# Performance work log

Hardware: AMD Instinct MI355X
Metric: run time of the kernel (lower is better)

## Reference

```python
import jax, jax.numpy as jnp
import numpy as np
from jax import lax

NEG = -1e30  # safe -inf surrogate (avoids inf-inf NaNs under vjp)


def setup_inputs() -> dict:
    key = jax.random.key(0)
    k1, k2, k3, k4 = jax.random.split(key, 4)
    B, T, U, V = 8, 128, 64, 1024
    acts = jax.random.normal(k1, (B, T, U + 1, V), dtype=jnp.float32)
    # labels in [1, V): blank (0) never appears in target sequences
    labels = jax.random.randint(k2, (B, U), 1, V, dtype=jnp.int32)
    act_lens = jax.random.randint(k3, (B,), T // 2, T + 1, dtype=jnp.int32)
    label_lens = jax.random.randint(k4, (B,), U // 2, U + 1, dtype=jnp.int32)
    return {"acts": acts, "labels": labels, "act_lens": act_lens, "label_lens": label_lens}


def _rnnt_costs(acts, labels, act_lens, label_lens, blank=0):
    """Per-example negative log-likelihood of the RNNT alignment lattice.
    acts: (B, T, U+1, V) logits (warp_rnnt applies log_softmax internally).
    """
    B, T, U1, V = acts.shape
    U = U1 - 1
    lp = jax.nn.log_softmax(acts, axis=-1)
    lp_blank = lp[..., blank]                                        # (B, T, U+1)
    lab = jnp.broadcast_to(labels[:, None, :, None], (B, T, U, 1))
    lp_label = jnp.take_along_axis(lp[:, :, :U, :], lab, axis=3)[..., 0]  # (B, T, U)
    # mask label emissions beyond each example's label length
    umask = jnp.arange(U)[None, :] < label_lens[:, None]             # (B, U)
    lp_label = jnp.where(umask[:, None, :], lp_label, NEG)

    def compute_row(fb, lt):
        # fb: (B, U+1) alpha[t-1, u] + lp_blank[t-1, u] (the "from below" term)
        # lt: (B, U)   label log-probs at time t
        # new[u] = logaddexp(fb[u], new[u-1] + lt[u-1])  -- sequential in u
        def u_step(carry, x):
            fb_u, lt_u = x
            new = jnp.logaddexp(fb_u, carry + lt_u)
            return new, new
        _, rest = lax.scan(u_step, fb[:, 0], (fb[:, 1:].T, lt.T))    # (U, B)
        return jnp.concatenate([fb[:, 0:1], rest.T], axis=1)         # (B, U+1)

    # t = 0 row: alpha[0,0] = 0; only label transitions along u
    fb0 = jnp.concatenate([jnp.zeros((B, 1), acts.dtype), jnp.full((B, U), NEG, acts.dtype)], axis=1)
    row0 = compute_row(fb0, lp_label[:, 0, :])

    def t_step(prev_row, x):
        lpb_prev, lt = x
        row = compute_row(prev_row + lpb_prev, lt)
        return row, row

    xs = (jnp.moveaxis(lp_blank[:, :-1, :], 0, 1),   # (T-1, B, U+1)
          jnp.moveaxis(lp_label[:, 1:, :], 0, 1))    # (T-1, B, U)
    _, rows = lax.scan(t_step, row0, xs)             # (T-1, B, U+1)
    alphas = jnp.concatenate([row0[None], rows], axis=0)  # (T, B, U+1)

    b = jnp.arange(B)
    tl = act_lens - 1
    final = alphas[tl, b, label_lens] + lp_blank[b, tl, label_lens]
    return -final                                     # (B,)


def reference(acts, labels, act_lens, label_lens):
    # matches torch module defaults: size_average=False, blank_label=0
    costs = _rnnt_costs(acts, labels, act_lens, label_lens, blank=0)
    return jnp.sum(costs).reshape(1)
```

## Files before the change

kernel.cpp:

```cpp
#include <hip/hip_runtime.h>

#define LN2F 0.6931471805599453f

#define B_   8
#define T_   128
#define U_   64
#define U1_  65
#define V_   1024
#define ROWS_ (B_*T_*U1_)
#define NDIAG_ 224
#define DS_    66
#define PACKB_ (NDIAG_*DS_)
#define COL0N_ 224
#define NWAVES_ 8192
#define K1_BLOCKS_ 2048

typedef float f32x4 __attribute__((ext_vector_type(4)));

__device__ __forceinline__ float shr1_f32(float x) {
  return __int_as_float(__builtin_amdgcn_update_dpp(
      0, __float_as_int(x), 0x138, 0xf, 0xf, true));
}

__device__ __forceinline__ int wave_max_bexp(float a, float i0) {
  int e  = (int)((__float_as_uint(a)  >> 23) & 0xffu);
  int e2 = (int)((__float_as_uint(i0) >> 23) & 0xffu);
  e = max(e, e2);
  int t;
  t = __builtin_amdgcn_update_dpp(e, e, 0x111, 0xf, 0xf, false); e = max(e, t);
  t = __builtin_amdgcn_update_dpp(e, e, 0x112, 0xf, 0xf, false); e = max(e, t);
  t = __builtin_amdgcn_update_dpp(e, e, 0x114, 0xf, 0xf, false); e = max(e, t);
  t = __builtin_amdgcn_update_dpp(e, e, 0x118, 0xf, 0xf, false); e = max(e, t);
  t = __builtin_amdgcn_update_dpp(e, e, 0x142, 0xf, 0xf, false); e = max(e, t);
  t = __builtin_amdgcn_update_dpp(e, e, 0x143, 0xf, 0xf, false); e = max(e, t);
  return __builtin_amdgcn_readlane(e, 63);
}

__global__ __launch_bounds__(256) void k1_linsoftmax(
    const float* __restrict__ acts, const int* __restrict__ labels,
    const int* __restrict__ label_lens,
    float2* __restrict__ pack, float2* __restrict__ col0, int* __restrict__ cnt) {
  const int lane = threadIdx.x & 63;
  const int wid  = blockIdx.x * 4 + (threadIdx.x >> 6);
  if (wid == 0 && lane == 0) *cnt = 0;

  for (int row = wid; row < ROWS_; row += NWAVES_) {
    const int b   = row / (T_ * U1_);
    const int rem = row - b * (T_ * U1_);
    const int t   = rem / U1_;
    const int u   = rem - t * U1_;
    const float* __restrict__ p = acts + (size_t)row * V_;

    int ll_ = 0; float labv = 0.0f;
    if (lane == 0 && u < U_) {
      ll_  = label_lens[b];
      labv = p[labels[b * U_ + u]];
    }

    f32x4 v0 = *(const f32x4*)(p +   0 + lane * 4);
    f32x4 v1 = *(const f32x4*)(p + 256 + lane * 4);
    f32x4 v2 = *(const f32x4*)(p + 512 + lane * 4);
    f32x4 v3 = *(const f32x4*)(p + 768 + lane * 4);

    float m = fmaxf(fmaxf(fmaxf(v0.x, v0.y), fmaxf(v0.z, v0.w)),
              fmaxf(fmaxf(fmaxf(v1.x, v1.y), fmaxf(v1.z, v1.w)),
              fmaxf(fmaxf(fmaxf(v2.x, v2.y), fmaxf(v2.z, v2.w)),
                    fmaxf(fmaxf(v3.x, v3.y), fmaxf(v3.z, v3.w)))));
    #pragma unroll
    for (int o = 32; o; o >>= 1) m = fmaxf(m, __shfl_xor(m, o, 64));

    float e00 = __expf(v0.x - m);
    float s = e00          + __expf(v0.y - m) + __expf(v0.z - m) + __expf(v0.w - m)
            + __expf(v1.x - m) + __expf(v1.y - m) + __expf(v1.z - m) + __expf(v1.w - m)
            + __expf(v2.x - m) + __expf(v2.y - m) + __expf(v2.z - m) + __expf(v2.w - m)
            + __expf(v3.x - m) + __expf(v3.y - m) + __expf(v3.z - m) + __expf(v3.w - m);
    #pragma unroll
    for (int o = 32; o; o >>= 1) s += __shfl_xor(s, o, 64);

    if (lane == 0) {
      float rs = 1.0f / s;
      float pb = e00 * rs;
      float2* pk = pack + (size_t)b * PACKB_;
      if (u == 0) {
        float pl0 = __expf(labv - m) * rs;
        col0[b * COL0N_ + (t + 1)] = make_float2(pb, pl0);
        pk[(size_t)(t + 1) * DS_ + 1].x = pl0;
      } else {
        pk[(size_t)(t + u) * DS_ + u].y = pb;
        if (u < U_) {
          float plv = (u < ll_) ? (__expf(labv - m) * rs) : 0.0f;
          pk[(size_t)(t + u + 1) * DS_ + (u + 1)].x = plv;
        }
      }
    }
  }
}

__global__ __launch_bounds__(64) void k2_alpha(
    const float2* __restrict__ pack, const float2* __restrict__ col0,
    const int* __restrict__ act_lens, const int* __restrict__ label_lens,
    float* __restrict__ costs, int* __restrict__ cnt, float* __restrict__ out) {
  const int b  = (int)blockIdx.x;
  const int l  = (int)threadIdx.x;
  const int tl = act_lens[b] - 1;
  const int ll = label_lens[b];
  const int u  = l + 1;
  const int tcap = (u == ll) ? tl : 0x7fffffff;

  const float2* __restrict__ pku = pack + (size_t)b * PACKB_ + u;
  const float2* __restrict__ c0  = col0 + (size_t)b * COL0N_;

  float a = 0.0f;
  float i0 = (l == 0) ? 1.0f : 0.0f;
  float fin = 0.0f, pbc = 0.0f;
  int   S = 0, Ecap = 0;
  int   t_ = -u;

  float2 pA[16], pB[16], cA[16], cB[16];

#define LOADP(P, C, DB) do {                                             \
    const float2* q_ = pku + (size_t)(DB) * DS_;                         \
    _Pragma("unroll")                                                    \
    for (int j = 0; j < 16; ++j) (P)[j] = q_[(size_t)j * DS_];           \
    _Pragma("unroll")                                                    \
    for (int j = 0; j < 16; ++j) {                                       \
      float2 cv_ = c0[(DB) + j];                                         \
      bool ok_ = ((DB) + j) <= T_;                  \
      (C)[j].x = ok_ ? cv_.x : 0.0f;                                     \
      (C)[j].y = ok_ ? cv_.y : 0.0f;                                     \
    }                                                                    \
  } while (0)

#define RENORM() do {                                                    \
    int eS_ = wave_max_bexp(a, i0);                                      \
    int sh_ = min(167 - eS_, 126);     \
    S += sh_;                                                            \
    float sc_ = ldexpf(1.0f, sh_);                                       \
    a *= sc_; i0 *= sc_;                                                 \
  } while (0)

#define COMPUTE8(P, C, JO) do {                                          \
    _Pragma("unroll")                                                    \
    for (int jj = 0; jj < 8; ++jj) {                                     \
      const int j = (JO) + jj;                                           \
      t_ += 1;                                                           \
      float shin = shr1_f32(a);                                          \
      float inj  = i0 * (C)[j].y;                                        \
      float anew = fmaf(a, pbc, fmaf(shin, (P)[j].x, inj));              \
      bool valid = ((unsigned)t_ < (unsigned)T_);                        \
      a = valid ? anew : 0.0f;                \
      bool cap = (t_ == tcap);                                           \
      fin  = cap ? a : fin;                                              \
      Ecap = cap ? S : Ecap;                                             \
      i0 *= (C)[j].x;                                                    \
      pbc = (P)[j].y;                                                    \
    }                                                                    \
  } while (0)

  LOADP(pA, cA, 1);
  #pragma unroll 1
  for (int it = 0; it < 12; it += 2) {
    LOADP(pB, cB, 16 * it + 17);
    if (it > 0) RENORM();
    COMPUTE8(pA, cA, 0);
    RENORM();
    COMPUTE8(pA, cA, 8);
    if (it < 10) LOADP(pA, cA, 16 * it + 33);
    RENORM();
    COMPUTE8(pB, cB, 0);
    RENORM();
    COMPUTE8(pB, cB, 8);
  }
#undef LOADP
#undef RENORM
#undef COMPUTE8

  if (u == ll) {
    float pblast = pack[(size_t)b * PACKB_ + (size_t)(tl + ll) * DS_ + ll].y;
    float lg = __log2f(fin) - (float)Ecap + __log2f(pblast);
    costs[b] = -lg * LN2F;
  }

  __threadfence();
  if (l == 0) {
    int old = atomicAdd(cnt, 1);
    if (old == B_ - 1) {
      __threadfence();
      volatile const float* vc = costs;
      float s = 0.0f;
      #pragma unroll
      for (int i = 0; i < B_; ++i) s += vc[i];
      out[0] = s;
    }
  }
}

extern "C" void kernel_launch(void* const* d_in, const int* in_sizes, int n_in,
                              void* d_out, int out_size, void* d_ws, size_t ws_size,
                              hipStream_t stream) {
  const float* acts       = (const float*)d_in[0];
  const int*   labels     = (const int*)d_in[1];
  const int*   act_lens   = (const int*)d_in[2];
  const int*   label_lens = (const int*)d_in[3];

  float2* pack  = (float2*)d_ws;
  float2* col0  = pack + (size_t)B_ * PACKB_;
  float*  costs = (float*)(col0 + (size_t)B_ * COL0N_);
  int*    cnt   = (int*)(costs + B_);

  k1_linsoftmax<<<K1_BLOCKS_, 256, 0, stream>>>(acts, labels, label_lens, pack, col0, cnt);
  k2_alpha<<<B_, 64, 0, stream>>>(pack, col0, act_lens, label_lens, costs, cnt, (float*)d_out);
}
```

Measured before the change: 61.61 us.

## Give softmax waves contiguous row chunks and reduce costs in one alpha block

The softmax kernel now gives each wave a contiguous chunk of 13 rows and steps (b,t,u) incrementally, so the per-row integer divisions and the strided grid loop go away. Since 1280 blocks × 4 waves × 13 rows equals exactly B*T*(U+1), the chunks cover every row with no tail check. The alpha kernel runs as a single 512-thread block with one wave per batch element and sums the costs through shared memory. This replaces the global atomic counter, the thread fences and the workspace reset in the first kernel. In exchange, all 8 recurrences share one workgroup on one CU, and the fixed chunk size ties the code to these exact shapes.

New measurement: 72.72 us. +18.0%, slower.

```diff
diff --git a/kernel.cpp b/kernel.cpp
--- a/kernel.cpp
+++ b/kernel.cpp
@@ -12,8 +12,8 @@
 #define DS_    66
 #define PACKB_ (NDIAG_*DS_)
 #define COL0N_ 224
-#define NWAVES_ 8192
-#define K1_BLOCKS_ 2048
+#define RPW_   13
+#define K1_BLOCKS_ 1280
 
 typedef float f32x4 __attribute__((ext_vector_type(4)));
 
@@ -39,18 +39,19 @@
 __global__ __launch_bounds__(256) void k1_linsoftmax(
     const float* __restrict__ acts, const int* __restrict__ labels,
     const int* __restrict__ label_lens,
-    float2* __restrict__ pack, float2* __restrict__ col0, int* __restrict__ cnt) {
+    float2* __restrict__ pack, float2* __restrict__ col0) {
   const int lane = threadIdx.x & 63;
   const int wid  = blockIdx.x * 4 + (threadIdx.x >> 6);
-  if (wid == 0 && lane == 0) *cnt = 0;
-
-  for (int row = wid; row < ROWS_; row += NWAVES_) {
-    const int b   = row / (T_ * U1_);
-    const int rem = row - b * (T_ * U1_);
-    const int t   = rem / U1_;
-    const int u   = rem - t * U1_;
-    const float* __restrict__ p = acts + (size_t)row * V_;
-
+
+  int row = wid * RPW_;
+  int b   = row / (T_ * U1_);
+  int rem = row - b * (T_ * U1_);
+  int t   = rem / U1_;
+  int u   = rem - t * U1_;
+  const float* p = acts + (size_t)row * V_;
+
+  #pragma unroll 1
+  for (int i = 0; i < RPW_; ++i) {
     int ll_ = 0; float labv = 0.0f;
     if (lane == 0 && u < U_) {
       ll_  = label_lens[b];
@@ -93,15 +94,22 @@
         }
       }
     }
-  }
-}
-
-__global__ __launch_bounds__(64) void k2_alpha(
+
+    if (i < RPW_ - 1) {
+      p += V_;
+      if (++u == U1_) { u = 0; if (++t == T_) { t = 0; ++b; } }
+    }
+  }
+}
+
+__global__ __launch_bounds__(512) void k2_alpha(
     const float2* __restrict__ pack, const float2* __restrict__ col0,
     const int* __restrict__ act_lens, const int* __restrict__ label_lens,
-    float* __restrict__ costs, int* __restrict__ cnt, float* __restrict__ out) {
-  const int b  = (int)blockIdx.x;
-  const int l  = (int)threadIdx.x;
+    float* __restrict__ out) {
+  __shared__ float costs_s[B_];
+  const int w  = (int)threadIdx.x >> 6;
+  const int l  = (int)threadIdx.x & 63;
+  const int b  = w;
   const int tl = act_lens[b] - 1;
   const int ll = label_lens[b];
   const int u  = l + 1;
@@ -178,20 +186,14 @@
   if (u == ll) {
     float pblast = pack[(size_t)b * PACKB_ + (size_t)(tl + ll) * DS_ + ll].y;
     float lg = __log2f(fin) - (float)Ecap + __log2f(pblast);
-    costs[b] = -lg * LN2F;
-  }
-
-  __threadfence();
-  if (l == 0) {
-    int old = atomicAdd(cnt, 1);
-    if (old == B_ - 1) {
-      __threadfence();
-      volatile const float* vc = costs;
-      float s = 0.0f;
-      #pragma unroll
-      for (int i = 0; i < B_; ++i) s += vc[i];
-      out[0] = s;
-    }
+    costs_s[b] = -lg * LN2F;
+  }
+  __syncthreads();
+  if (threadIdx.x == 0) {
+    float s = 0.0f;
+    #pragma unroll
+    for (int i = 0; i < B_; ++i) s += costs_s[i];
+    out[0] = s;
   }
 }
 
@@ -203,11 +205,9 @@
   const int*   act_lens   = (const int*)d_in[2];
   const int*   label_lens = (const int*)d_in[3];
 
-  float2* pack  = (float2*)d_ws;
-  float2* col0  = pack + (size_t)B_ * PACKB_;
-  float*  costs = (float*)(col0 + (size_t)B_ * COL0N_);
-  int*    cnt   = (int*)(costs + B_);
-
-  k1_linsoftmax<<<K1_BLOCKS_, 256, 0, stream>>>(acts, labels, label_lens, pack, col0, cnt);
-  k2_alpha<<<B_, 64, 0, stream>>>(pack, col0, act_lens, label_lens, costs, cnt, (float*)d_out);
-}
+  float2* pack = (float2*)d_ws;
+  float2* col0 = pack + (size_t)B_ * PACKB_;
+
+  k1_linsoftmax<<<K1_BLOCKS_, 256, 0, stream>>>(acts, labels, label_lens, pack, col0);
+  k2_alpha<<<1, 512, 0, stream>>>(pack, col0, act_lens, label_lens, (float*)d_out);
+}
```
